# Performance work log

Measured on AMD Instinct MI355X. Metric: run time of the kernel, lower is better.

## Reference

```python
import jax, jax.numpy as jnp
import numpy as np

SELF_IMPORTANCE = 0.25  # blend weight for the node's own transformed features


def setup_inputs() -> dict:
    key = jax.random.key(0)
    k1, k2, k3, k4, k5 = jax.random.split(key, 5)
    F, newF, N = 128, 64, 500000
    return {
        "x": jax.random.normal(k1, (1, F), dtype=jnp.float32),
        "X": jax.random.normal(k2, (N, F), dtype=jnp.float32),
        "kernel": jax.random.normal(k3, (F, newF), dtype=jnp.float32) * (1.0 / np.sqrt(F)),
        "attn_self": jax.random.normal(k4, (newF, 1), dtype=jnp.float32) * (1.0 / np.sqrt(newF)),
        "attn_neigh": jax.random.normal(k5, (newF, 1), dtype=jnp.float32) * (1.0 / np.sqrt(newF)),
    }


def reference(x, X, kernel, attn_self, attn_neigh):
    # x: [1, F] node features; X: [N, F] neighbor features
    x_t = x @ kernel            # [1, newF]
    X_t = X @ kernel            # [N, newF]
    a_self = x_t @ attn_self    # [1, 1]
    a_neigh = X_t @ attn_neigh  # [N, 1]
    # repeat_elements(a_self, N) + a_neigh, then transpose -> [1, N]
    scores = (a_self + a_neigh).T
    # original adds mask = exp(-1e10) * -1e10 == -0.0 (a no-op); faithful softmax:
    attn = jax.nn.softmax(scores, axis=-1)  # [1, N]
    # Dropout is identity at inference (eval mode)
    feats_neigh = attn @ X_t    # [1, newF]
    return (1.0 - SELF_IMPORTANCE) * feats_neigh + SELF_IMPORTANCE * x_t
```

## Files before the change

### kernel.cpp

```cpp
#include <hip/hip_runtime.h>
#include <math.h>


#define TPB 512
#define MAXBLK 512
#define PART_STRIDE 136
#define PART_BASE 256

__global__ __launch_bounds__(128) void gat_prep(
    const float* __restrict__ x, const float* __restrict__ kern,
    const float* __restrict__ attn_neigh, float* __restrict__ ws) {
  int t = threadIdx.x;
  float s = 0.f;
#pragma unroll 8
  for (int c = 0; c < 64; ++c) s += kern[t * 64 + c] * attn_neigh[c];
  ws[t] = s;
  if (t < 64) {
    float s2 = 0.f;
#pragma unroll 8
    for (int j = 0; j < 128; ++j) s2 += x[j] * kern[j * 64 + t];
    ws[128 + t] = s2;
  }
}

__global__ __launch_bounds__(TPB) void gat_main(
    const float4* __restrict__ X4, const float* __restrict__ ws,
    float* __restrict__ part, int N, int npairs, int totalWaves) {
  const int lane = threadIdx.x & 63;
  const int half = lane >> 5;
  const int hl = lane & 31;
  const int wid = threadIdx.x >> 6;
  const int gwave = blockIdx.x * (TPB / 64) + wid;

  const float4 wv = ((const float4*)ws)[hl];

  float m = -INFINITY, l = 0.f;
  float ax = 0.f, ay = 0.f, az = 0.f, aw = 0.f;

  for (int p = gwave; p < npairs; p += totalWaves) {
    const bool ok = (2 * p + half) < N;
    float4 xv = make_float4(0.f, 0.f, 0.f, 0.f);
    if (ok) xv = X4[(size_t)p * 64 + lane];
    float s = xv.x * wv.x + xv.y * wv.y + xv.z * wv.z + xv.w * wv.w;
    s += __shfl_xor(s, 1);
    s += __shfl_xor(s, 2);
    s += __shfl_xor(s, 4);
    s += __shfl_xor(s, 8);
    s += __shfl_xor(s, 16);
    const float mn = ok ? fmaxf(m, s) : m;
    const float corr = (m == mn) ? 1.f : __expf(m - mn);
    const float pw = ok ? __expf(s - mn) : 0.f;
    l = l * corr + pw;
    ax = ax * corr + pw * xv.x;
    ay = ay * corr + pw * xv.y;
    az = az * corr + pw * xv.z;
    aw = aw * corr + pw * xv.w;
    m = mn;
  }

  const float m_o = __shfl_xor(m, 32);
  const float l_o = __shfl_xor(l, 32);
  const float axo = __shfl_xor(ax, 32);
  const float ayo = __shfl_xor(ay, 32);
  const float azo = __shfl_xor(az, 32);
  const float awo = __shfl_xor(aw, 32);
  const float M2 = fmaxf(m, m_o);
  const float c0 = (m == -INFINITY) ? 0.f : __expf(m - M2);
  const float c1 = (m_o == -INFINITY) ? 0.f : __expf(m_o - M2);
  const float l2 = l * c0 + l_o * c1;
  const float bx = ax * c0 + axo * c1;
  const float by = ay * c0 + ayo * c1;
  const float bz = az * c0 + azo * c1;
  const float bw = aw * c0 + awo * c1;

  __shared__ float sm[TPB / 64];
  __shared__ float sl[TPB / 64];
  __shared__ float sacc[TPB / 64][128];
  if (lane < 32) {
    sacc[wid][hl * 4 + 0] = bx;
    sacc[wid][hl * 4 + 1] = by;
    sacc[wid][hl * 4 + 2] = bz;
    sacc[wid][hl * 4 + 3] = bw;
    if (hl == 0) { sm[wid] = M2; sl[wid] = l2; }
  }
  __syncthreads();

  if (threadIdx.x < 32) {
    float Mb = -INFINITY;
#pragma unroll
    for (int w2 = 0; w2 < TPB / 64; ++w2) Mb = fmaxf(Mb, sm[w2]);
    float Lb = 0.f, fx = 0.f, fy = 0.f, fz = 0.f, fw = 0.f;
#pragma unroll
    for (int w2 = 0; w2 < TPB / 64; ++w2) {
      const float sc = (sm[w2] == -INFINITY) ? 0.f : __expf(sm[w2] - Mb);
      Lb += sc * sl[w2];
      fx += sc * sacc[w2][hl * 4 + 0];
      fy += sc * sacc[w2][hl * 4 + 1];
      fz += sc * sacc[w2][hl * 4 + 2];
      fw += sc * sacc[w2][hl * 4 + 3];
    }
    float* pb = part + (size_t)blockIdx.x * PART_STRIDE;
    if (hl == 0) { pb[0] = Mb; pb[1] = Lb; }
    float4 v = make_float4(fx, fy, fz, fw);
    ((float4*)(pb + 8))[hl] = v;
  }
}

__global__ __launch_bounds__(256) void gat_fin(
    const float* __restrict__ kern, const float* __restrict__ ws,
    float* __restrict__ out, int nblk) {
  __shared__ float scale[MAXBLK];
  __shared__ float red[256];
  __shared__ float feats[128];
  const int t = threadIdx.x;
  const float* part = ws + PART_BASE;

  float m = -INFINITY;
  for (int b = t; b < nblk; b += 256) m = fmaxf(m, part[(size_t)b * PART_STRIDE]);
  red[t] = m;
  __syncthreads();
  for (int s = 128; s > 0; s >>= 1) {
    if (t < s) red[t] = fmaxf(red[t], red[t + s]);
    __syncthreads();
  }
  const float M = red[0];
  __syncthreads();

  float lp = 0.f;
  for (int b = t; b < nblk; b += 256) {
    const float mb = part[(size_t)b * PART_STRIDE];
    const float sc = (mb == -INFINITY) ? 0.f : __expf(mb - M);
    scale[b] = sc;
    lp += sc * part[(size_t)b * PART_STRIDE + 1];
  }
  red[t] = lp;
  __syncthreads();
  for (int s = 128; s > 0; s >>= 1) {
    if (t < s) red[t] += red[t + s];
    __syncthreads();
  }
  const float L = red[0];
  __syncthreads();

  if (t < 128) {
    float f = 0.f;
    for (int b = 0; b < nblk; ++b) f += scale[b] * part[(size_t)b * PART_STRIDE + 8 + t];
    feats[t] = f / L;
  }
  __syncthreads();

  if (t < 64) {
    float s = 0.f;
#pragma unroll 8
    for (int j = 0; j < 128; ++j) s += feats[j] * kern[j * 64 + t];
    out[t] = 0.75f * s + 0.25f * ws[128 + t];
  }
}

extern "C" void kernel_launch(void* const* d_in, const int* in_sizes, int n_in,
                              void* d_out, int out_size, void* d_ws, size_t ws_size,
                              hipStream_t stream) {
  const float* x          = (const float*)d_in[0];
  const float* X          = (const float*)d_in[1];
  const float* kern       = (const float*)d_in[2];
  const float* attn_neigh = (const float*)d_in[4];
  float* ws  = (float*)d_ws;
  float* out = (float*)d_out;

  const int N = in_sizes[1] / 128;
  const int npairs = (N + 1) >> 1;

  int nblk = MAXBLK;
  const size_t availF = ws_size / 4;
  if (availF < (size_t)PART_BASE + (size_t)MAXBLK * PART_STRIDE) {
    long cap = ((long)availF - PART_BASE) / PART_STRIDE;
    nblk = (cap < 1) ? 1 : (int)cap;
  }
  const int totalWaves = nblk * (TPB / 64);

  gat_prep<<<1, 128, 0, stream>>>(x, kern, attn_neigh, ws);
  gat_main<<<nblk, TPB, 0, stream>>>((const float4*)X, ws, ws + PART_BASE,
                                     N, npairs, totalWaves);
  gat_fin<<<1, 256, 0, stream>>>(kern, ws, out, nblk);
}
```

Measured before the change: 391.1 us.

## Unroll main loop with two independent online-softmax streams and double the grid

The streaming loop now issues two row-pair loads per iteration and keeps two independent online-softmax accumulators, merging them at the end. This raises memory-level parallelism and breaks the serial dependency on the running max. The bounds checks leave the hot loop: an odd final row is handled by one wave, and the per-iteration conditionals on the rescale factor are removed. The block count doubles to 1024 and launch bounds request higher occupancy, which adds partials for the single-block finalize kernel to reduce.

```diff
diff --git a/kernel.cpp b/kernel.cpp
--- a/kernel.cpp
+++ b/kernel.cpp
@@ -3,7 +3,7 @@
 
 
 #define TPB 512
-#define MAXBLK 512
+#define MAXBLK 1024
 #define PART_STRIDE 136
 #define PART_BASE 256
 
@@ -23,9 +23,9 @@
   }
 }
 
-__global__ __launch_bounds__(TPB) void gat_main(
+__global__ __launch_bounds__(TPB, 6) void gat_main(
     const float4* __restrict__ X4, const float* __restrict__ ws,
-    float* __restrict__ part, int N, int npairs, int totalWaves) {
+    float* __restrict__ part, int N, int totalWaves) {
   const int lane = threadIdx.x & 63;
   const int half = lane >> 5;
   const int hl = lane & 31;
@@ -34,28 +34,82 @@
 
   const float4 wv = ((const float4*)ws)[hl];
 
-  float m = -INFINITY, l = 0.f;
-  float ax = 0.f, ay = 0.f, az = 0.f, aw = 0.f;
-
-  for (int p = gwave; p < npairs; p += totalWaves) {
-    const bool ok = (2 * p + half) < N;
+  const int npairs = N >> 1;
+
+  float mA = -INFINITY, lA = 0.f, aAx = 0.f, aAy = 0.f, aAz = 0.f, aAw = 0.f;
+  float mB = -INFINITY, lB = 0.f, aBx = 0.f, aBy = 0.f, aBz = 0.f, aBw = 0.f;
+
+  int p = gwave;
+  const int stride = totalWaves;
+  for (; p + stride < npairs; p += 2 * stride) {
+    const float4 xv0 = X4[(size_t)p * 64 + lane];
+    const float4 xv1 = X4[(size_t)(p + stride) * 64 + lane];
+
+    float s0 = xv0.x * wv.x + xv0.y * wv.y + xv0.z * wv.z + xv0.w * wv.w;
+    s0 += __shfl_xor(s0, 1);  s0 += __shfl_xor(s0, 2);  s0 += __shfl_xor(s0, 4);
+    s0 += __shfl_xor(s0, 8);  s0 += __shfl_xor(s0, 16);
+    {
+      const float mn = fmaxf(mA, s0);
+      const float corr = __expf(mA - mn);
+      const float pw = __expf(s0 - mn);
+      lA = lA * corr + pw;
+      aAx = aAx * corr + pw * xv0.x;  aAy = aAy * corr + pw * xv0.y;
+      aAz = aAz * corr + pw * xv0.z;  aAw = aAw * corr + pw * xv0.w;
+      mA = mn;
+    }
+    float s1 = xv1.x * wv.x + xv1.y * wv.y + xv1.z * wv.z + xv1.w * wv.w;
+    s1 += __shfl_xor(s1, 1);  s1 += __shfl_xor(s1, 2);  s1 += __shfl_xor(s1, 4);
+    s1 += __shfl_xor(s1, 8);  s1 += __shfl_xor(s1, 16);
+    {
+      const float mn = fmaxf(mB, s1);
+      const float corr = __expf(mB - mn);
+      const float pw = __expf(s1 - mn);
+      lB = lB * corr + pw;
+      aBx = aBx * corr + pw * xv1.x;  aBy = aBy * corr + pw * xv1.y;
+      aBz = aBz * corr + pw * xv1.z;  aBw = aBw * corr + pw * xv1.w;
+      mB = mn;
+    }
+  }
+  if (p < npairs) {
+    const float4 xv0 = X4[(size_t)p * 64 + lane];
+    float s0 = xv0.x * wv.x + xv0.y * wv.y + xv0.z * wv.z + xv0.w * wv.w;
+    s0 += __shfl_xor(s0, 1);  s0 += __shfl_xor(s0, 2);  s0 += __shfl_xor(s0, 4);
+    s0 += __shfl_xor(s0, 8);  s0 += __shfl_xor(s0, 16);
+    const float mn = fmaxf(mA, s0);
+    const float corr = __expf(mA - mn);
+    const float pw = __expf(s0 - mn);
+    lA = lA * corr + pw;
+    aAx = aAx * corr + pw * xv0.x;  aAy = aAy * corr + pw * xv0.y;
+    aAz = aAz * corr + pw * xv0.z;  aAw = aAw * corr + pw * xv0.w;
+    mA = mn;
+  }
+
+  if ((N & 1) && gwave == 0) {
     float4 xv = make_float4(0.f, 0.f, 0.f, 0.f);
-    if (ok) xv = X4[(size_t)p * 64 + lane];
+    if (half == 0) xv = X4[(size_t)(N - 1) * 32 + hl];
     float s = xv.x * wv.x + xv.y * wv.y + xv.z * wv.z + xv.w * wv.w;
-    s += __shfl_xor(s, 1);
-    s += __shfl_xor(s, 2);
-    s += __shfl_xor(s, 4);
-    s += __shfl_xor(s, 8);
-    s += __shfl_xor(s, 16);
-    const float mn = ok ? fmaxf(m, s) : m;
-    const float corr = (m == mn) ? 1.f : __expf(m - mn);
-    const float pw = ok ? __expf(s - mn) : 0.f;
-    l = l * corr + pw;
-    ax = ax * corr + pw * xv.x;
-    ay = ay * corr + pw * xv.y;
-    az = az * corr + pw * xv.z;
-    aw = aw * corr + pw * xv.w;
-    m = mn;
+    s += __shfl_xor(s, 1);  s += __shfl_xor(s, 2);  s += __shfl_xor(s, 4);
+    s += __shfl_xor(s, 8);  s += __shfl_xor(s, 16);
+    if (half == 0) {
+      const float mn = fmaxf(mA, s);
+      const float corr = __expf(mA - mn);
+      const float pw = __expf(s - mn);
+      lA = lA * corr + pw;
+      aAx = aAx * corr + pw * xv.x;  aAy = aAy * corr + pw * xv.y;
+      aAz = aAz * corr + pw * xv.z;  aAw = aAw * corr + pw * xv.w;
+      mA = mn;
+    }
+  }
+
+  float m, l, ax, ay, az, aw;
+  {
+    const float M = fmaxf(mA, mB);
+    const float cA = (mA == -INFINITY) ? 0.f : __expf(mA - M);
+    const float cB = (mB == -INFINITY) ? 0.f : __expf(mB - M);
+    l = lA * cA + lB * cB;
+    ax = aAx * cA + aBx * cB;  ay = aAy * cA + aBy * cB;
+    az = aAz * cA + aBz * cB;  aw = aAw * cA + aBw * cB;
+    m = M;
   }
 
   const float m_o = __shfl_xor(m, 32);
@@ -168,7 +222,6 @@
   float* out = (float*)d_out;
 
   const int N = in_sizes[1] / 128;
-  const int npairs = (N + 1) >> 1;
 
   int nblk = MAXBLK;
   const size_t availF = ws_size / 4;
@@ -180,6 +233,6 @@
 
   gat_prep<<<1, 128, 0, stream>>>(x, kern, attn_neigh, ws);
   gat_main<<<nblk, TPB, 0, stream>>>((const float4*)X, ws, ws + PART_BASE,
-                                     N, npairs, totalWaves);
+                                     N, totalWaves);
   gat_fin<<<1, 256, 0, stream>>>(kern, ws, out, nblk);
 }
```

Result: slower. 432.0 us (+10.5%).

## Prefetch next row pair in streaming softmax loop and widen grid

Applied to the files above, without the earlier changes.

The main streaming kernel now loads the next pair of rows before processing the current one, a software prefetch that keeps more loads in flight. The per-iteration bounds checks are removed, and an odd trailing row is handled separately by wave 0. The grid changes from 512 blocks of 512 threads to 2048 blocks of 256 threads with an occupancy hint. The final reduction kernel is widened to 512 threads and splits the feature accumulation over four block groups to absorb the larger number of partials. The tradeoffs are higher register pressure and more partials for the final kernel to combine.

```diff
diff --git a/kernel.cpp b/kernel.cpp
--- a/kernel.cpp
+++ b/kernel.cpp
@@ -2,10 +2,11 @@
 #include <math.h>
 
 
-#define TPB 512
-#define MAXBLK 512
+#define TPB 256
+#define MAXBLK 2048
 #define PART_STRIDE 136
 #define PART_BASE 256
+#define FIN_TPB 512
 
 __global__ __launch_bounds__(128) void gat_prep(
     const float* __restrict__ x, const float* __restrict__ kern,
@@ -23,9 +24,9 @@
   }
 }
 
-__global__ __launch_bounds__(TPB) void gat_main(
+__global__ __launch_bounds__(TPB, 8) void gat_main(
     const float4* __restrict__ X4, const float* __restrict__ ws,
-    float* __restrict__ part, int N, int npairs, int totalWaves) {
+    float* __restrict__ part, int N, int totalWaves) {
   const int lane = threadIdx.x & 63;
   const int half = lane >> 5;
   const int hl = lane & 31;
@@ -34,28 +35,60 @@
 
   const float4 wv = ((const float4*)ws)[hl];
 
+  const int npairs = N >> 1;
+  const int stride = totalWaves;
+
   float m = -INFINITY, l = 0.f;
   float ax = 0.f, ay = 0.f, az = 0.f, aw = 0.f;
 
-  for (int p = gwave; p < npairs; p += totalWaves) {
-    const bool ok = (2 * p + half) < N;
-    float4 xv = make_float4(0.f, 0.f, 0.f, 0.f);
-    if (ok) xv = X4[(size_t)p * 64 + lane];
+  int p = gwave;
+  float4 xv = make_float4(0.f, 0.f, 0.f, 0.f);
+  if (p < npairs) xv = X4[(size_t)p * 64 + lane];
+
+  for (; p + stride < npairs; p += stride) {
+    const float4 xn = X4[(size_t)(p + stride) * 64 + lane];
+
     float s = xv.x * wv.x + xv.y * wv.y + xv.z * wv.z + xv.w * wv.w;
-    s += __shfl_xor(s, 1);
-    s += __shfl_xor(s, 2);
-    s += __shfl_xor(s, 4);
-    s += __shfl_xor(s, 8);
-    s += __shfl_xor(s, 16);
-    const float mn = ok ? fmaxf(m, s) : m;
-    const float corr = (m == mn) ? 1.f : __expf(m - mn);
-    const float pw = ok ? __expf(s - mn) : 0.f;
+    s += __shfl_xor(s, 1);  s += __shfl_xor(s, 2);  s += __shfl_xor(s, 4);
+    s += __shfl_xor(s, 8);  s += __shfl_xor(s, 16);
+    const float mn = fmaxf(m, s);
+    const float corr = __expf(m - mn);
+    const float pw = __expf(s - mn);
     l = l * corr + pw;
-    ax = ax * corr + pw * xv.x;
-    ay = ay * corr + pw * xv.y;
-    az = az * corr + pw * xv.z;
-    aw = aw * corr + pw * xv.w;
+    ax = ax * corr + pw * xv.x;  ay = ay * corr + pw * xv.y;
+    az = az * corr + pw * xv.z;  aw = aw * corr + pw * xv.w;
     m = mn;
+
+    xv = xn;
+  }
+  if (p < npairs) {
+    float s = xv.x * wv.x + xv.y * wv.y + xv.z * wv.z + xv.w * wv.w;
+    s += __shfl_xor(s, 1);  s += __shfl_xor(s, 2);  s += __shfl_xor(s, 4);
+    s += __shfl_xor(s, 8);  s += __shfl_xor(s, 16);
+    const float mn = fmaxf(m, s);
+    const float corr = __expf(m - mn);
+    const float pw = __expf(s - mn);
+    l = l * corr + pw;
+    ax = ax * corr + pw * xv.x;  ay = ay * corr + pw * xv.y;
+    az = az * corr + pw * xv.z;  aw = aw * corr + pw * xv.w;
+    m = mn;
+  }
+
+  if ((N & 1) && gwave == 0) {
+    float4 tv = make_float4(0.f, 0.f, 0.f, 0.f);
+    if (half == 0) tv = X4[(size_t)(N - 1) * 32 + hl];
+    float s = tv.x * wv.x + tv.y * wv.y + tv.z * wv.z + tv.w * wv.w;
+    s += __shfl_xor(s, 1);  s += __shfl_xor(s, 2);  s += __shfl_xor(s, 4);
+    s += __shfl_xor(s, 8);  s += __shfl_xor(s, 16);
+    if (half == 0) {
+      const float mn = fmaxf(m, s);
+      const float corr = __expf(m - mn);
+      const float pw = __expf(s - mn);
+      l = l * corr + pw;
+      ax = ax * corr + pw * tv.x;  ay = ay * corr + pw * tv.y;
+      az = az * corr + pw * tv.z;  aw = aw * corr + pw * tv.w;
+      m = mn;
+    }
   }
 
   const float m_o = __shfl_xor(m, 32);
@@ -106,20 +139,21 @@
   }
 }
 
-__global__ __launch_bounds__(256) void gat_fin(
+__global__ __launch_bounds__(FIN_TPB) void gat_fin(
     const float* __restrict__ kern, const float* __restrict__ ws,
     float* __restrict__ out, int nblk) {
   __shared__ float scale[MAXBLK];
-  __shared__ float red[256];
+  __shared__ float red[FIN_TPB];
+  __shared__ float fpart[4][128];
   __shared__ float feats[128];
   const int t = threadIdx.x;
   const float* part = ws + PART_BASE;
 
   float m = -INFINITY;
-  for (int b = t; b < nblk; b += 256) m = fmaxf(m, part[(size_t)b * PART_STRIDE]);
+  for (int b = t; b < nblk; b += FIN_TPB) m = fmaxf(m, part[(size_t)b * PART_STRIDE]);
   red[t] = m;
   __syncthreads();
-  for (int s = 128; s > 0; s >>= 1) {
+  for (int s = FIN_TPB / 2; s > 0; s >>= 1) {
     if (t < s) red[t] = fmaxf(red[t], red[t + s]);
     __syncthreads();
   }
@@ -127,7 +161,7 @@
   __syncthreads();
 
   float lp = 0.f;
-  for (int b = t; b < nblk; b += 256) {
+  for (int b = t; b < nblk; b += FIN_TPB) {
     const float mb = part[(size_t)b * PART_STRIDE];
     const float sc = (mb == -INFINITY) ? 0.f : __expf(mb - M);
     scale[b] = sc;
@@ -135,18 +169,22 @@
   }
   red[t] = lp;
   __syncthreads();
-  for (int s = 128; s > 0; s >>= 1) {
+  for (int s = FIN_TPB / 2; s > 0; s >>= 1) {
     if (t < s) red[t] += red[t + s];
     __syncthreads();
   }
   const float L = red[0];
   __syncthreads();
 
-  if (t < 128) {
+  {
+    const int j = t & 127;
+    const int q = t >> 7;
     float f = 0.f;
-    for (int b = 0; b < nblk; ++b) f += scale[b] * part[(size_t)b * PART_STRIDE + 8 + t];
-    feats[t] = f / L;
-  }
+    for (int b = q; b < nblk; b += 4) f += scale[b] * part[(size_t)b * PART_STRIDE + 8 + j];
+    fpart[q][j] = f;
+  }
+  __syncthreads();
+  if (t < 128) feats[t] = (fpart[0][t] + fpart[1][t] + fpart[2][t] + fpart[3][t]) / L;
   __syncthreads();
 
   if (t < 64) {
@@ -168,7 +206,6 @@
   float* out = (float*)d_out;
 
   const int N = in_sizes[1] / 128;
-  const int npairs = (N + 1) >> 1;
 
   int nblk = MAXBLK;
   const size_t availF = ws_size / 4;
@@ -180,6 +217,6 @@
 
   gat_prep<<<1, 128, 0, stream>>>(x, kern, attn_neigh, ws);
   gat_main<<<nblk, TPB, 0, stream>>>((const float4*)X, ws, ws + PART_BASE,
-                                     N, npairs, totalWaves);
-  gat_fin<<<1, 256, 0, stream>>>(kern, ws, out, nblk);
-}
+                                     N, totalWaves);
+  gat_fin<<<1, FIN_TPB, 0, stream>>>(kern, ws, out, nblk);
+}
```

Measured after the change: 484.6 us. 1.24x slower.
